# Optimization experiments

Hardware: AMD Instinct MI355X
Metric: run time of the kernel (lower is better)

## Reference

```python
import jax, jax.numpy as jnp
import numpy as np

N_NODES = 50000
N_EDGES = 600000
IN_CH = 128
HID_CH = 128


def setup_inputs() -> dict:
    key = jax.random.key(0)
    ks = jax.random.split(key, 8)
    x = jax.random.normal(ks[0], (N_NODES, IN_CH), dtype=jnp.float32)
    edge_index = jax.random.randint(ks[1], (2, N_EDGES), 0, N_NODES, dtype=jnp.int64)
    # Glorot-style scaling for weights, zero bias (PyG GCNConv defaults)
    def glorot(k, fi, fo):
        lim = (6.0 / (fi + fo)) ** 0.5
        return jax.random.uniform(k, (fi, fo), minval=-lim, maxval=lim, dtype=jnp.float32)
    return {
        "x": x,
        "edge_index": edge_index,
        "W_base": glorot(ks[2], IN_CH, HID_CH),
        "b_base": jnp.zeros((HID_CH,), jnp.float32),
        "W_mu": glorot(ks[3], HID_CH, IN_CH),
        "b_mu": jnp.zeros((IN_CH,), jnp.float32),
        "W_logstd": glorot(ks[4], HID_CH, IN_CH),
        "b_logstd": jnp.zeros((IN_CH,), jnp.float32),
    }


def _gcn_norm(edge_index, n_nodes):
    # PyG gcn_norm: add self-loops, symmetric normalization D^-1/2 A D^-1/2
    loop = jnp.arange(n_nodes, dtype=edge_index.dtype)
    src = jnp.concatenate([edge_index[0], loop])  # [E + N]
    dst = jnp.concatenate([edge_index[1], loop])
    deg = jnp.zeros((n_nodes,), jnp.float32).at[dst].add(1.0)
    dinv = jnp.where(deg > 0, jax.lax.rsqrt(deg), 0.0)
    norm = dinv[src] * dinv[dst]  # [E + N]
    return src, dst, norm


def _gcn_conv(x, src, dst, norm, W, b, n_nodes):
    xw = x @ W                          # [N, F_out] dense linear
    msg = xw[src] * norm[:, None]       # gather + scale over edges
    out = jax.ops.segment_sum(msg, dst, num_segments=n_nodes)  # scatter-add
    return out + b


def reference(x, edge_index, W_base, b_base, W_mu, b_mu, W_logstd, b_logstd):
    n_nodes = x.shape[0]
    src, dst, norm = _gcn_norm(edge_index, n_nodes)
    h = _gcn_conv(x, src, dst, norm, W_base, b_base, n_nodes)
    m = jax.nn.relu(_gcn_conv(h, src, dst, norm, W_mu, b_mu, n_nodes))
    s = jax.nn.relu(_gcn_conv(h, src, dst, norm, W_logstd, b_logstd, n_nodes))
    return (m, s)
```

## Files before the change

kernel.cpp:

```cpp
#include <hip/hip_runtime.h>
#include <hip/hip_fp16.h>


#define CH 128
#define SCAN_CHUNK 1024

typedef __attribute__((ext_vector_type(8))) _Float16 half8v;
typedef __attribute__((ext_vector_type(16))) float floatx16;

__global__ void count_kernel(const int* __restrict__ ei, int E, int* __restrict__ cnt) {
  int e = blockIdx.x * blockDim.x + threadIdx.x;
  if (e < E) atomicAdd(&cnt[ei[E + e]], 1);
}

__global__ __launch_bounds__(256) void scan1p_kernel(const int* __restrict__ cnt,
    int n, int nb, int* __restrict__ gsum, int* __restrict__ flags,
    int* __restrict__ rowptr, int* __restrict__ cursor, float* __restrict__ dinv) {
  __shared__ int sthr[256];
  __shared__ int soff;
  int bid = blockIdx.x;
  int base = bid * SCAN_CHUNK;
  int tid = threadIdx.x;
  int v[4];
  int ts = 0;
  #pragma unroll
  for (int j = 0; j < 4; ++j) {
    int i = base + tid * 4 + j;
    v[j] = (i < n) ? cnt[i] : 0;
    ts += v[j];
  }
  sthr[tid] = ts;
  if (tid == 0) soff = 0;
  __syncthreads();
  for (int off = 1; off < 256; off <<= 1) {
    int t = (tid >= off) ? sthr[tid - off] : 0;
    __syncthreads();
    sthr[tid] += t;
    __syncthreads();
  }
  int blocksum = sthr[255];
  if (tid == 0) {
    gsum[bid] = blocksum;
    __threadfence();
    atomicExch(&flags[bid], 1);
  }
  for (int j = tid; j < bid; j += 256) {
    while (atomicAdd(&flags[j], 0) == 0) {}
    atomicAdd(&soff, atomicAdd(&gsum[j], 0));
  }
  __syncthreads();
  int offset = soff;
  int excl = sthr[tid] - ts + offset;
  #pragma unroll
  for (int j = 0; j < 4; ++j) {
    int i = base + tid * 4 + j;
    if (i < n) {
      rowptr[i] = excl;
      cursor[i] = excl;
      dinv[i]   = rsqrtf((float)(v[j] + 1));
      excl += v[j];
    }
  }
  if (bid == nb - 1 && tid == 0) rowptr[n] = offset + blocksum;
}

__global__ void fill_kernel(const int* __restrict__ ei, int E,
                            int* __restrict__ cursor, int* __restrict__ col) {
  int e = blockIdx.x * blockDim.x + threadIdx.x;
  if (e < E) {
    int d = ei[E + e];
    int pos = atomicAdd(&cursor[d], 1);
    col[pos] = ei[e];
  }
}

__global__ __launch_bounds__(256) void mega1_kernel(
    const float* __restrict__ x, ushort* __restrict__ xh, int n8,
    int* __restrict__ cnt, int ncnt4, int* __restrict__ flags,
    const float* __restrict__ Wb, const float* __restrict__ bb,
    const float* __restrict__ Wmu, const float* __restrict__ Wls,
    ushort* __restrict__ Wcmh, ushort* __restrict__ Wcml,
    ushort* __restrict__ Wcsh, ushort* __restrict__ Wcsl,
    float* __restrict__ pm, float* __restrict__ ps) {
  int gid = blockIdx.x;
  int tid = threadIdx.x;
  if (gid < 32) {
    int sel = gid >> 4;
    const float* W2 = sel ? Wls : Wmu;
    ushort* Wh = sel ? Wcsh : Wcmh;
    ushort* Wl = sel ? Wcsl : Wcml;
    int o = (gid & 15) * 1024 + tid * 4;
    int k = o >> 7, c = o & 127;
    float acc[4] = {0.f, 0.f, 0.f, 0.f};
    for (int j = 0; j < 128; ++j) {
      float a = Wb[k * 128 + j];
      const float* wr = &W2[j * 128 + c];
      acc[0] = fmaf(a, wr[0], acc[0]);
      acc[1] = fmaf(a, wr[1], acc[1]);
      acc[2] = fmaf(a, wr[2], acc[2]);
      acc[3] = fmaf(a, wr[3], acc[3]);
    }
    #pragma unroll
    for (int j = 0; j < 4; ++j) {
      _Float16 h = (_Float16)acc[j];
      float resid = acc[j] - (float)h;
      _Float16 l = (_Float16)resid;
      Wh[(c + j) * 128 + k] = __builtin_bit_cast(ushort, h);
      Wl[(c + j) * 128 + k] = __builtin_bit_cast(ushort, l);
    }
  } else if (gid == 32) {
    if (tid < 16) ((int4*)flags)[tid] = make_int4(0, 0, 0, 0);
    int sel = tid >> 7, c = tid & 127;
    const float* W2 = sel ? Wls : Wmu;
    float acc = 0.f;
    for (int j = 0; j < 128; ++j) acc = fmaf(bb[j], W2[j * 128 + c], acc);
    (sel ? ps : pm)[c] = acc;
  } else {
    int t = (gid - 33) * 256 + tid;
    if (t < ncnt4) ((int4*)cnt)[t] = make_int4(0, 0, 0, 0);
    if (t < n8) {
      const float4* f4 = (const float4*)x;
      float4 a = f4[2 * t], b = f4[2 * t + 1];
      __half h[8] = {__float2half_rn(a.x), __float2half_rn(a.y),
                     __float2half_rn(a.z), __float2half_rn(a.w),
                     __float2half_rn(b.x), __float2half_rn(b.y),
                     __float2half_rn(b.z), __float2half_rn(b.w)};
      ((uint4*)xh)[t] = *(const uint4*)h;
    }
  }
}

__device__ inline void h8_fma(uint4 v, float s, float* a) {
  const __half2* h2 = (const __half2*)&v;
  #pragma unroll
  for (int i = 0; i < 4; ++i) {
    float2 f = __half22float2(h2[i]);
    a[2 * i]     = fmaf(s, f.x, a[2 * i]);
    a[2 * i + 1] = fmaf(s, f.y, a[2 * i + 1]);
  }
}

__global__ __launch_bounds__(256) void agg_kernel(const ushort* __restrict__ feat,
    const int* __restrict__ rowptr, const int* __restrict__ col,
    const float* __restrict__ dinv,
    ushort* __restrict__ out_h, float* __restrict__ r_out, int n) {
  int w = (blockIdx.x * 256 + threadIdx.x) >> 6;
  if (w >= n) return;
  int lane = threadIdx.x & 63;
  int g  = lane >> 4;
  int cl = lane & 15;
  const uint4* u4 = (const uint4*)feat;
  float di = dinv[w];
  float a[8] = {0.f, 0.f, 0.f, 0.f, 0.f, 0.f, 0.f, 0.f};
  float rsum = 0.f;
  if (g == 0) {
    h8_fma(u4[(size_t)w * 16 + cl], di, a);
  }
  int s = rowptr[w], e = rowptr[w + 1];
  int j = s;
  for (; j + 16 <= e; j += 16) {
    int c0 = col[j + g];
    int c1 = col[j + 4 + g];
    int c2 = col[j + 8 + g];
    int c3 = col[j + 12 + g];
    float s0 = dinv[c0], s1 = dinv[c1], s2 = dinv[c2], s3 = dinv[c3];
    rsum += (s0 + s1) + (s2 + s3);
    uint4 v0 = u4[(size_t)c0 * 16 + cl];
    uint4 v1 = u4[(size_t)c1 * 16 + cl];
    uint4 v2 = u4[(size_t)c2 * 16 + cl];
    uint4 v3 = u4[(size_t)c3 * 16 + cl];
    h8_fma(v0, s0, a);
    h8_fma(v1, s1, a);
    h8_fma(v2, s2, a);
    h8_fma(v3, s3, a);
  }
  for (; j + 8 <= e; j += 8) {
    int c0 = col[j + g];
    int c1 = col[j + 4 + g];
    float s0 = dinv[c0], s1 = dinv[c1];
    rsum += s0 + s1;
    uint4 v0 = u4[(size_t)c0 * 16 + cl];
    uint4 v1 = u4[(size_t)c1 * 16 + cl];
    h8_fma(v0, s0, a);
    h8_fma(v1, s1, a);
  }
  for (; j < e; j += 4) {
    int jj = j + g;
    if (jj < e) {
      int c = col[jj];
      float s0 = dinv[c];
      rsum += s0;
      h8_fma(u4[(size_t)c * 16 + cl], s0, a);
    }
  }
  #pragma unroll
  for (int m = 16; m <= 32; m <<= 1) {
    #pragma unroll
    for (int i = 0; i < 8; ++i) a[i] += __shfl_xor(a[i], m);
    rsum += __shfl_xor(rsum, m);
  }
  if (g == 0) {
    __half h[8];
    #pragma unroll
    for (int i = 0; i < 8; ++i) h[i] = __float2half_rn(a[i] * di);
    ((uint4*)out_h)[(size_t)w * 16 + cl] = *(const uint4*)h;
    if (r_out && cl == 0) r_out[w] = di * (di + rsum);
  }
}

__global__ __launch_bounds__(256) void gemm_mfma_kernel(
    const ushort* __restrict__ Ah16,
    const ushort* __restrict__ W0h, const ushort* __restrict__ W0l,
    const float* __restrict__ p0, const float* __restrict__ b0,
    const ushort* __restrict__ W1h, const ushort* __restrict__ W1l,
    const float* __restrict__ p1, const float* __restrict__ b1,
    const float* __restrict__ rbuf,
    float* __restrict__ out0, float* __restrict__ out1,
    int M) {
  __shared__ ushort Wh[64 * 128];
  __shared__ ushort Wl[64 * 128];

  const int mat = blockIdx.y >> 1;
  const int c0  = (blockIdx.y & 1) * 64;
  const uint4* GH = (const uint4*)(mat ? W1h : W0h);
  const uint4* GL = (const uint4*)(mat ? W1l : W0l);
  const float* pp = mat ? p1 : p0;
  const float* bb = mat ? b1 : b0;
  float*     outp = mat ? out1 : out0;

  const int tid  = threadIdx.x;
  const int lane = tid & 63;
  const int wv   = tid >> 6;
  const int rA   = lane & 31;
  const int kh   = lane >> 5;
  const int row  = blockIdx.x * 128 + wv * 32 + rA;
  const bool rowok = row < M;

  {
    uint4* LH = (uint4*)Wh;
    uint4* LL = (uint4*)Wl;
    #pragma unroll
    for (int t = 0; t < 4; ++t) {
      int q = tid + t * 256;
      int wr = q >> 4, ls = q & 15;
      int phys = ls ^ (wr & 15);
      LH[wr * 16 + phys] = GH[(c0 + wr) * 16 + ls];
      LL[wr * 16 + phys] = GL[(c0 + wr) * 16 + ls];
    }
  }

  const uint4* AH = (const uint4*)Ah16;
  const uint4 zero4 = make_uint4(0, 0, 0, 0);

  half8v ah[8];
  #pragma unroll
  for (int kc = 0; kc < 8; ++kc) {
    uint4 v = rowok ? AH[row * 16 + kc * 2 + kh] : zero4;
    ah[kc] = __builtin_bit_cast(half8v, v);
  }

  __syncthreads();

  floatx16 acc[2];
  #pragma unroll
  for (int t = 0; t < 2; ++t)
    #pragma unroll
    for (int j = 0; j < 16; ++j) acc[t][j] = 0.f;

  const uint4* WHv = (const uint4*)Wh;
  const uint4* WLv = (const uint4*)Wl;

  #pragma unroll
  for (int kc = 0; kc < 8; ++kc) {
    int fk = kc * 2 + kh;
    int ph = fk ^ (rA & 15);
    half8v wh[2], wl[2];
    #pragma unroll
    for (int t = 0; t < 2; ++t) {
      wh[t] = __builtin_bit_cast(half8v, WHv[(t * 32 + rA) * 16 + ph]);
      wl[t] = __builtin_bit_cast(half8v, WLv[(t * 32 + rA) * 16 + ph]);
    }
    #pragma unroll
    for (int t = 0; t < 2; ++t)
      acc[t] = __builtin_amdgcn_mfma_f32_32x32x16_f16(ah[kc], wh[t], acc[t], 0, 0, 0);
    #pragma unroll
    for (int t = 0; t < 2; ++t)
      acc[t] = __builtin_amdgcn_mfma_f32_32x32x16_f16(ah[kc], wl[t], acc[t], 0, 0, 0);
  }

  float bcol[2], pcol[2];
  #pragma unroll
  for (int t = 0; t < 2; ++t) {
    bcol[t] = bb[c0 + t * 32 + rA];
    pcol[t] = pp[c0 + t * 32 + rA];
  }
  #pragma unroll
  for (int r = 0; r < 16; ++r) {
    int r32 = (r & 3) + 8 * (r >> 2) + 4 * kh;
    int orow = blockIdx.x * 128 + wv * 32 + r32;
    if (orow < M) {
      float rb = rbuf[orow];
      #pragma unroll
      for (int t = 0; t < 2; ++t) {
        float v = acc[t][r] + fmaf(rb, pcol[t], bcol[t]);
        v = fmaxf(v, 0.f);
        outp[(size_t)orow * CH + c0 + t * 32 + rA] = v;
      }
    }
  }
}

extern "C" void kernel_launch(void* const* d_in, const int* in_sizes, int n_in,
                              void* d_out, int out_size, void* d_ws, size_t ws_size,
                              hipStream_t stream) {
  const float* x      = (const float*)d_in[0];
  const int*   ei     = (const int*)d_in[1];
  const float* W_base = (const float*)d_in[2];
  const float* b_base = (const float*)d_in[3];
  const float* W_mu   = (const float*)d_in[4];
  const float* b_mu   = (const float*)d_in[5];
  const float* W_ls   = (const float*)d_in[6];
  const float* b_ls   = (const float*)d_in[7];
  float* out = (float*)d_out;

  const int N = in_sizes[0] / CH;
  const int E = in_sizes[1] / 2;

  char* ws = (char*)d_ws;
  size_t off = 0;
  auto carve = [&](size_t bytes) -> void* {
    void* p = ws + off;
    off += (bytes + 511) & ~(size_t)511;
    return p;
  };
  int*    cnt    = (int*)carve((size_t)N * 4);
  int*    rowptr = (int*)carve((size_t)(N + 1) * 4);
  int*    cursor = (int*)carve((size_t)N * 4);
  int*    col    = (int*)carve((size_t)E * 4);
  float*  dinv   = (float*)carve((size_t)N * 4);
  float*  rbuf   = (float*)carve((size_t)N * 4);
  int*    gsum   = (int*)carve((size_t)64 * 4);
  int*    flags  = (int*)carve((size_t)64 * 4);
  float*  pm   = (float*)carve((size_t)CH * 4);
  float*  ps   = (float*)carve((size_t)CH * 4);
  ushort* Wcmh = (ushort*)carve((size_t)CH * CH * 2);
  ushort* Wcml = (ushort*)carve((size_t)CH * CH * 2);
  ushort* Wcsh = (ushort*)carve((size_t)CH * CH * 2);
  ushort* Wcsl = (ushort*)carve((size_t)CH * CH * 2);
  ushort* xh   = (ushort*)carve((size_t)N * CH * 2);
  ushort* t1h  = (ushort*)carve((size_t)N * CH * 2);
  ushort* zh   = (ushort*)carve((size_t)N * CH * 2);

  int eb = (E + 255) / 256;
  int nb = (N + SCAN_CHUNK - 1) / SCAN_CHUNK;
  int n8 = N * CH / 8;
  int ncnt4 = (N + 3) / 4;

  mega1_kernel<<<33 + (n8 + 255) / 256, 256, 0, stream>>>(
      x, xh, n8, cnt, ncnt4, flags,
      W_base, b_base, W_mu, W_ls, Wcmh, Wcml, Wcsh, Wcsl, pm, ps);
  count_kernel<<<eb, 256, 0, stream>>>(ei, E, cnt);
  scan1p_kernel<<<nb, 256, 0, stream>>>(cnt, N, nb, gsum, flags,
                                        rowptr, cursor, dinv);
  fill_kernel<<<eb, 256, 0, stream>>>(ei, E, cursor, col);

  int ab = (N * 64 + 255) / 256;
  int gb = (N + 127) / 128;

  agg_kernel<<<ab, 256, 0, stream>>>(xh, rowptr, col, dinv, t1h, nullptr, N);
  agg_kernel<<<ab, 256, 0, stream>>>(t1h, rowptr, col, dinv, zh, rbuf, N);
  gemm_mfma_kernel<<<dim3(gb, 4), 256, 0, stream>>>(zh,
                                           Wcmh, Wcml, pm, b_mu,
                                           Wcsh, Wcsl, ps, b_ls,
                                           rbuf, out, out + (size_t)N * CH, N);
}
```

Measured before the change: 163.8 us.

## Fuse CSR count, scan and fill into one persistent kernel with grid barriers

```diff
diff --git a/kernel.cpp b/kernel.cpp
--- a/kernel.cpp
+++ b/kernel.cpp
@@ -4,79 +4,99 @@
 
 #define CH 128
 #define SCAN_CHUNK 1024
+#define CSR_BLOCKS 1024
 
 typedef __attribute__((ext_vector_type(8))) _Float16 half8v;
 typedef __attribute__((ext_vector_type(16))) float floatx16;
 
-__global__ void count_kernel(const int* __restrict__ ei, int E, int* __restrict__ cnt) {
-  int e = blockIdx.x * blockDim.x + threadIdx.x;
-  if (e < E) atomicAdd(&cnt[ei[E + e]], 1);
-}
-
-__global__ __launch_bounds__(256) void scan1p_kernel(const int* __restrict__ cnt,
-    int n, int nb, int* __restrict__ gsum, int* __restrict__ flags,
-    int* __restrict__ rowptr, int* __restrict__ cursor, float* __restrict__ dinv) {
-  __shared__ int sthr[256];
-  __shared__ int soff;
-  int bid = blockIdx.x;
-  int base = bid * SCAN_CHUNK;
-  int tid = threadIdx.x;
-  int v[4];
-  int ts = 0;
-  #pragma unroll
-  for (int j = 0; j < 4; ++j) {
-    int i = base + tid * 4 + j;
-    v[j] = (i < n) ? cnt[i] : 0;
-    ts += v[j];
-  }
-  sthr[tid] = ts;
-  if (tid == 0) soff = 0;
+__device__ inline void gbar(int* ctr, int nblocks) {
   __syncthreads();
-  for (int off = 1; off < 256; off <<= 1) {
-    int t = (tid >= off) ? sthr[tid - off] : 0;
+  if (threadIdx.x == 0) {
+    __threadfence();
+    __hip_atomic_fetch_add(ctr, 1, __ATOMIC_ACQ_REL, __HIP_MEMORY_SCOPE_AGENT);
+    while (__hip_atomic_load(ctr, __ATOMIC_ACQUIRE, __HIP_MEMORY_SCOPE_AGENT)
+           < nblocks) {}
+  }
+  __syncthreads();
+}
+
+__global__ __launch_bounds__(256) void csr_kernel(
+    const int* __restrict__ ei, int E, int n, int nb_chunks,
+    int* __restrict__ cnt, int* __restrict__ gsum, int* __restrict__ flags,
+    int* __restrict__ bar,
+    int* __restrict__ rowptr, int* __restrict__ cursor,
+    float* __restrict__ dinv, int* __restrict__ col) {
+  const int bid = blockIdx.x;
+  const int tid = threadIdx.x;
+  const int stride = CSR_BLOCKS * 256;
+
+  for (int e = bid * 256 + tid; e < E; e += stride)
+    atomicAdd(&cnt[ei[E + e]], 1);
+
+  gbar(&bar[0], CSR_BLOCKS);
+
+  if (bid < nb_chunks) {
+    __shared__ int sthr[256];
+    __shared__ int soff;
+    int base = bid * SCAN_CHUNK;
+    int v[4];
+    int ts = 0;
+    #pragma unroll
+    for (int j = 0; j < 4; ++j) {
+      int i = base + tid * 4 + j;
+      v[j] = (i < n) ? cnt[i] : 0;
+      ts += v[j];
+    }
+    sthr[tid] = ts;
+    if (tid == 0) soff = 0;
     __syncthreads();
-    sthr[tid] += t;
+    for (int off = 1; off < 256; off <<= 1) {
+      int t = (tid >= off) ? sthr[tid - off] : 0;
+      __syncthreads();
+      sthr[tid] += t;
+      __syncthreads();
+    }
+    int blocksum = sthr[255];
+    if (tid == 0) {
+      gsum[bid] = blocksum;
+      __threadfence();
+      __hip_atomic_store(&flags[bid], 1, __ATOMIC_RELEASE,
+                         __HIP_MEMORY_SCOPE_AGENT);
+    }
+    for (int j = tid; j < bid; j += 256) {
+      while (__hip_atomic_load(&flags[j], __ATOMIC_ACQUIRE,
+                               __HIP_MEMORY_SCOPE_AGENT) == 0) {}
+      atomicAdd(&soff, gsum[j]);
+    }
     __syncthreads();
-  }
-  int blocksum = sthr[255];
-  if (tid == 0) {
-    gsum[bid] = blocksum;
-    __threadfence();
-    atomicExch(&flags[bid], 1);
-  }
-  for (int j = tid; j < bid; j += 256) {
-    while (atomicAdd(&flags[j], 0) == 0) {}
-    atomicAdd(&soff, atomicAdd(&gsum[j], 0));
-  }
-  __syncthreads();
-  int offset = soff;
-  int excl = sthr[tid] - ts + offset;
-  #pragma unroll
-  for (int j = 0; j < 4; ++j) {
-    int i = base + tid * 4 + j;
-    if (i < n) {
-      rowptr[i] = excl;
-      cursor[i] = excl;
-      dinv[i]   = rsqrtf((float)(v[j] + 1));
-      excl += v[j];
-    }
-  }
-  if (bid == nb - 1 && tid == 0) rowptr[n] = offset + blocksum;
-}
-
-__global__ void fill_kernel(const int* __restrict__ ei, int E,
-                            int* __restrict__ cursor, int* __restrict__ col) {
-  int e = blockIdx.x * blockDim.x + threadIdx.x;
-  if (e < E) {
+    int offset = soff;
+    int excl = sthr[tid] - ts + offset;
+    #pragma unroll
+    for (int j = 0; j < 4; ++j) {
+      int i = base + tid * 4 + j;
+      if (i < n) {
+        rowptr[i] = excl;
+        cursor[i] = excl;
+        dinv[i]   = rsqrtf((float)(v[j] + 1));
+        excl += v[j];
+      }
+    }
+    if (bid == nb_chunks - 1 && tid == 0) rowptr[n] = offset + blocksum;
+  }
+
+  gbar(&bar[1], CSR_BLOCKS);
+
+  for (int e = bid * 256 + tid; e < E; e += stride) {
     int d = ei[E + e];
     int pos = atomicAdd(&cursor[d], 1);
-    col[pos] = ei[e];
+    __builtin_nontemporal_store(ei[e], &col[pos]);
   }
 }
 
 __global__ __launch_bounds__(256) void mega1_kernel(
     const float* __restrict__ x, ushort* __restrict__ xh, int n8,
     int* __restrict__ cnt, int ncnt4, int* __restrict__ flags,
+    int* __restrict__ bar,
     const float* __restrict__ Wb, const float* __restrict__ bb,
     const float* __restrict__ Wmu, const float* __restrict__ Wls,
     ushort* __restrict__ Wcmh, ushort* __restrict__ Wcml,
@@ -110,6 +130,7 @@
     }
   } else if (gid == 32) {
     if (tid < 16) ((int4*)flags)[tid] = make_int4(0, 0, 0, 0);
+    if (tid >= 16 && tid < 20) ((int4*)bar)[tid - 16] = make_int4(0, 0, 0, 0);
     int sel = tid >> 7, c = tid & 127;
     const float* W2 = sel ? Wls : Wmu;
     float acc = 0.f;
@@ -341,6 +362,7 @@
   float*  rbuf   = (float*)carve((size_t)N * 4);
   int*    gsum   = (int*)carve((size_t)64 * 4);
   int*    flags  = (int*)carve((size_t)64 * 4);
+  int*    bar    = (int*)carve((size_t)16 * 4);
   float*  pm   = (float*)carve((size_t)CH * 4);
   float*  ps   = (float*)carve((size_t)CH * 4);
   ushort* Wcmh = (ushort*)carve((size_t)CH * CH * 2);
@@ -351,18 +373,15 @@
   ushort* t1h  = (ushort*)carve((size_t)N * CH * 2);
   ushort* zh   = (ushort*)carve((size_t)N * CH * 2);
 
-  int eb = (E + 255) / 256;
   int nb = (N + SCAN_CHUNK - 1) / SCAN_CHUNK;
   int n8 = N * CH / 8;
   int ncnt4 = (N + 3) / 4;
 
   mega1_kernel<<<33 + (n8 + 255) / 256, 256, 0, stream>>>(
-      x, xh, n8, cnt, ncnt4, flags,
+      x, xh, n8, cnt, ncnt4, flags, bar,
       W_base, b_base, W_mu, W_ls, Wcmh, Wcml, Wcsh, Wcsl, pm, ps);
-  count_kernel<<<eb, 256, 0, stream>>>(ei, E, cnt);
-  scan1p_kernel<<<nb, 256, 0, stream>>>(cnt, N, nb, gsum, flags,
-                                        rowptr, cursor, dinv);
-  fill_kernel<<<eb, 256, 0, stream>>>(ei, E, cursor, col);
+  csr_kernel<<<CSR_BLOCKS, 256, 0, stream>>>(ei, E, N, nb, cnt, gsum, flags,
+                                             bar, rowptr, cursor, dinv, col);
 
   int ab = (N * 64 + 255) / 256;
   int gb = (N + 127) / 128;
```

After: 323.3 us. +97.4%, slower.
